# Performance work log

Measured on AMD Instinct MI355X. Metric: run time of the kernel, lower is better.

## Reference

```python
import jax, jax.numpy as jnp
import numpy as np
from jax import lax

B, N, W, L, H = 8, 1024, 1024, 12, 16
EPS = 1e-5


def setup_inputs() -> dict:
    key = jax.random.key(0)
    ks = jax.random.split(key, 14)
    std = 0.25 / np.sqrt(W)  # init_scale * sqrt(1/width)
    inp = {
        "x": jax.random.normal(ks[0], (B, N, W), dtype=jnp.float32),
        # stacked per-layer params, leading dim L
        "ln1_g": jnp.ones((L, W), jnp.float32),
        "ln1_b": jnp.zeros((L, W), jnp.float32),
        "w_qkv": jax.random.normal(ks[1], (L, W, 3 * W), jnp.float32) * std,
        "b_qkv": jnp.zeros((L, 3 * W), jnp.float32),
        "w_o":   jax.random.normal(ks[2], (L, W, W), jnp.float32) * std,
        "b_o":   jnp.zeros((L, W), jnp.float32),
        "ln2_g": jnp.ones((L, W), jnp.float32),
        "ln2_b": jnp.zeros((L, W), jnp.float32),
        "w_fc":  jax.random.normal(ks[3], (L, W, 4 * W), jnp.float32) * std,
        "b_fc":  jnp.zeros((L, 4 * W), jnp.float32),
        "w_pr":  jax.random.normal(ks[4], (L, 4 * W, W), jnp.float32) * std,
        "b_pr":  jnp.zeros((L, W), jnp.float32),
    }
    return inp


def _layernorm(x, g, b):
    mu = jnp.mean(x, axis=-1, keepdims=True)
    var = jnp.mean(jnp.square(x - mu), axis=-1, keepdims=True)
    return (x - mu) * lax.rsqrt(var + EPS) * g + b


def _attention(qkv, heads):
    # qkv: [B, N, 3W]; matches QKVMultiheadAttention exactly
    bs, n_ctx, width3 = qkv.shape
    attn_ch = width3 // heads // 3
    scale = 1.0 / np.sqrt(np.sqrt(attn_ch))
    qkv = qkv.reshape(bs, n_ctx, heads, 3 * attn_ch)
    q, k, v = jnp.split(qkv, 3, axis=-1)  # each [B,N,H,c]
    w = jnp.einsum("bthc,bshc->bhts", q * scale, k * scale)
    w = jax.nn.softmax(w.astype(jnp.float32), axis=-1).astype(qkv.dtype)
    out = jnp.einsum("bhts,bshc->bthc", w, v)
    return out.reshape(bs, n_ctx, heads * attn_ch)


def reference(x, ln1_g, ln1_b, w_qkv, b_qkv, w_o, b_o,
              ln2_g, ln2_b, w_fc, b_fc, w_pr, b_pr):
    params = (ln1_g, ln1_b, w_qkv, b_qkv, w_o, b_o,
              ln2_g, ln2_b, w_fc, b_fc, w_pr, b_pr)

    def step(h, p):
        (g1, bb1, wqkv, bqkv, wo, bo, g2, bb2, wfc, bfc, wpr, bpr) = p
        a = _layernorm(h, g1, bb1)
        a = jnp.einsum("bnw,wk->bnk", a, wqkv) + bqkv
        a = _attention(a, H)
        a = jnp.einsum("bnw,wk->bnk", a, wo) + bo
        h = h + a
        m = _layernorm(h, g2, bb2)
        m = jax.nn.gelu(jnp.einsum("bnw,wf->bnf", m, wfc) + bfc, approximate=False)
        m = jnp.einsum("bnf,fw->bnw", m, wpr) + bpr
        return h + m, None

    out, _ = lax.scan(step, x, params)
    return out
```

## Files before the change

kernel.cpp:

```cpp
#include <hip/hip_runtime.h>
#include <cstdint>
#include <cstddef>

#define WDIM 1024
#define BDIM 8
#define NDIM 1024
#define LDIM 12
#define HDIM 16
#define MROWS (BDIM * NDIM)

using bf16x8 = __attribute__((ext_vector_type(8))) __bf16;
using f32x4  = __attribute__((ext_vector_type(4))) float;
using u32x4  = __attribute__((ext_vector_type(4))) uint32_t;
using u16x8  = __attribute__((ext_vector_type(8))) ushort;

static __device__ __forceinline__ f32x4 mfma16(bf16x8 a, bf16x8 b, f32x4 c) {
  return __builtin_amdgcn_mfma_f32_16x16x32_bf16(a, b, c, 0, 0, 0);
}

static __device__ __forceinline__ ushort f2bf(float f) {
  uint32_t u = __builtin_bit_cast(uint32_t, f);
  u = (u + 0x7FFFu + ((u >> 16) & 1u)) >> 16;
  return (ushort)u;
}

static __device__ __forceinline__ uint32_t cvtpk(float lo, float hi) {
  uint32_t r;
  asm("v_cvt_pk_bf16_f32 %0, %1, %2" : "=v"(r) : "v"(lo), "v"(hi));
  return r;
}

static __device__ __forceinline__ void g2lds16(const void* g, void* l) {
  __builtin_amdgcn_global_load_lds(
      (__attribute__((address_space(1))) void*)(g),
      (__attribute__((address_space(3))) void*)(l), 16, 0, 0);
}

__global__ __launch_bounds__(256) void ln_kernel(const float* __restrict__ h,
                                                 const float* __restrict__ g,
                                                 const float* __restrict__ b,
                                                 ushort* __restrict__ out) {
  const int w = threadIdx.x >> 6, l = threadIdx.x & 63;
  const int row = blockIdx.x * 4 + w;
  const float4* rp = (const float4*)(h + (size_t)row * WDIM);
  float4 v[4];
  float s = 0.f, s2 = 0.f;
  #pragma unroll
  for (int j = 0; j < 4; ++j) {
    v[j] = rp[j * 64 + l];
    s  += v[j].x + v[j].y + v[j].z + v[j].w;
    s2 += v[j].x * v[j].x + v[j].y * v[j].y + v[j].z * v[j].z + v[j].w * v[j].w;
  }
  #pragma unroll
  for (int off = 32; off; off >>= 1) {
    s  += __shfl_xor(s, off);
    s2 += __shfl_xor(s2, off);
  }
  const float mu   = s * (1.0f / WDIM);
  const float var  = s2 * (1.0f / WDIM) - mu * mu;
  const float rstd = rsqrtf(var + 1e-5f);
  ushort4* op = (ushort4*)(out + (size_t)row * WDIM);
  #pragma unroll
  for (int j = 0; j < 4; ++j) {
    const float4 gv = ((const float4*)g)[j * 64 + l];
    const float4 bv = ((const float4*)b)[j * 64 + l];
    ushort4 o;
    o.x = f2bf((v[j].x - mu) * rstd * gv.x + bv.x);
    o.y = f2bf((v[j].y - mu) * rstd * gv.y + bv.y);
    o.z = f2bf((v[j].z - mu) * rstd * gv.z + bv.z);
    o.w = f2bf((v[j].w - mu) * rstd * gv.w + bv.w);
    op[j * 64 + l] = o;
  }
}

__global__ __launch_bounds__(256) void transpose_cvt(const float* __restrict__ in,
                                                     ushort* __restrict__ out,
                                                     int K, int N) {
  __shared__ float sm[32][33];
  const int n0 = blockIdx.x * 32, k0 = blockIdx.y * 32;
  const int tx = threadIdx.x, ty = threadIdx.y;
  #pragma unroll
  for (int j = 0; j < 4; ++j)
    sm[ty + j * 8][tx] = in[(size_t)(k0 + ty + j * 8) * N + n0 + tx];
  __syncthreads();
  #pragma unroll
  for (int j = 0; j < 4; ++j)
    out[(size_t)(n0 + ty + j * 8) * K + k0 + tx] = f2bf(sm[tx][ty + j * 8]);
}

__global__ __launch_bounds__(256) void v_transpose(const ushort* __restrict__ qkv,
                                                   ushort* __restrict__ vT) {
  const int nb = blockIdx.x, bh = blockIdx.y;
  const int b = bh >> 4, h = bh & 15;
  const int tid = threadIdx.x;
  __shared__ ushort smT[64 * 64];
  const int n0 = nb * 64;
  const size_t rowb = (size_t)b * NDIM;
  #pragma unroll
  for (int p = 0; p < 2; ++p) {
    const int n  = p * 32 + (tid >> 3);
    const int d0 = (tid & 7) * 8;
    const uint4 vv = *(const uint4*)(qkv + (rowb + n0 + n) * 3072 + h * 192 + 128 + d0);
    const ushort* e = (const ushort*)&vv;
    const int key = d0;
    #pragma unroll
    for (int j = 0; j < 8; ++j)
      smT[(d0 + j) * 64 + (n ^ key)] = e[j];
  }
  __syncthreads();
  #pragma unroll
  for (int p = 0; p < 2; ++p) {
    const int d  = p * 32 + (tid >> 3);
    const int nc = (tid & 7) * 8;
    const int key = (d >> 3) << 3;
    const uint4 ov = *(const uint4*)&smT[d * 64 + (nc ^ key)];
    *(uint4*)(vT + ((size_t)bh * 64 + d) * NDIM + n0 + nc) = ov;
  }
}

enum { EPI_BF16 = 0, EPI_RES = 1, EPI_GELU = 2 };

template <int EPI>
__global__ __launch_bounds__(512, 2) void gemm256_kernel(
    const ushort* __restrict__ A, const ushort* __restrict__ Bt,
    const float* __restrict__ bias, ushort* __restrict__ outb,
    int M, int N, int K) {
  __shared__ ushort smA[2 * 2 * 256 * 32];
  __shared__ ushort smB[2 * 2 * 256 * 32];
  const int tid = threadIdx.x;
  const int w = tid >> 6, l = tid & 63;
  const int lr = l & 15, lg = l >> 4;
  const int wm = w >> 2, wn = w & 3;

  const int gx = gridDim.x;
  const int nwg = gx * gridDim.y;
  const int id0 = blockIdx.y * gx + blockIdx.x;
  const int id = (id0 & 7) * (nwg >> 3) + (id0 >> 3);
  const int row0 = (id / gx) * 256, col0 = (id % gx) * 256;

  const int KT = K >> 6;
  const int srow_l = l >> 2;
  const int scol = (((l & 3) ^ ((l >> 3) & 3)) * 8);
  const int ks = ((lg ^ ((lr >> 1) & 3)) * 8);

  f32x4 acc[8][4] = {};

  auto stageA = [&](int tau, int hh) {
    const int base = (((tau & 1) * 2 + hh) * 8192);
    const int colb = tau * 64 + hh * 32 + scol;
    #pragma unroll
    for (int j = 0; j < 2; ++j) {
      const int c = j * 8 + w;
      g2lds16(A + (size_t)(row0 + 16 * c + srow_l) * K + colb, &smA[base + c * 512]);
    }
  };
  auto stageB = [&](int tau, int hh) {
    const int base = (((tau & 1) * 2 + hh) * 8192);
    const int colb = tau * 64 + hh * 32 + scol;
    #pragma unroll
    for (int j = 0; j < 2; ++j) {
      const int c = j * 8 + w;
      g2lds16(Bt + (size_t)(col0 + 16 * c + srow_l) * K + colb, &smB[base + c * 512]);
    }
  };

  stageA(0, 0); stageB(0, 0);
  stageA(0, 1); stageB(0, 1);
  stageA(1, 0); stageB(1, 0);
  asm volatile("s_waitcnt vmcnt(8)" ::: "memory");
  __builtin_amdgcn_sched_barrier(0);
  __builtin_amdgcn_s_barrier();

  for (int tau = 0; tau < KT; ++tau) {
    const int ab0 = (tau & 1) * 16384;
    const int ab1 = ab0 + 8192;
    bf16x8 af[8], bf0, bf1;

    #pragma unroll
    for (int m = 0; m < 8; ++m)
      af[m] = *(const bf16x8*)&smA[ab0 + (wm * 128 + m * 16 + lr) * 32 + ks];
    bf0 = *(const bf16x8*)&smB[ab0 + (wn * 64 + lr) * 32 + ks];
    bf1 = *(const bf16x8*)&smB[ab0 + (wn * 64 + 16 + lr) * 32 + ks];
    if (tau + 1 < KT) stageA(tau + 1, 1);
    __builtin_amdgcn_s_barrier();
    asm volatile("s_waitcnt lgkmcnt(0)" ::: "memory");
    __builtin_amdgcn_sched_barrier(0);
    __builtin_amdgcn_s_setprio(1);
    #pragma unroll
    for (int m = 0; m < 8; ++m) {
      acc[m][0] = mfma16(af[m], bf0, acc[m][0]);
      acc[m][1] = mfma16(af[m], bf1, acc[m][1]);
    }
    __builtin_amdgcn_s_setprio(0);
    __builtin_amdgcn_s_barrier();

    bf0 = *(const bf16x8*)&smB[ab0 + (wn * 64 + 32 + lr) * 32 + ks];
    bf1 = *(const bf16x8*)&smB[ab0 + (wn * 64 + 48 + lr) * 32 + ks];
    if (tau + 1 < KT) stageB(tau + 1, 1);
    __builtin_amdgcn_s_barrier();
    asm volatile("s_waitcnt lgkmcnt(0)" ::: "memory");
    __builtin_amdgcn_sched_barrier(0);
    __builtin_amdgcn_s_setprio(1);
    #pragma unroll
    for (int m = 0; m < 8; ++m) {
      acc[m][2] = mfma16(af[m], bf0, acc[m][2]);
      acc[m][3] = mfma16(af[m], bf1, acc[m][3]);
    }
    __builtin_amdgcn_s_setprio(0);
    if (tau + 1 < KT) { asm volatile("s_waitcnt vmcnt(8)" ::: "memory"); }
    else              { asm volatile("s_waitcnt vmcnt(0)" ::: "memory"); }
    __builtin_amdgcn_sched_barrier(0);
    __builtin_amdgcn_s_barrier();

    #pragma unroll
    for (int m = 0; m < 8; ++m)
      af[m] = *(const bf16x8*)&smA[ab1 + (wm * 128 + m * 16 + lr) * 32 + ks];
    bf0 = *(const bf16x8*)&smB[ab1 + (wn * 64 + lr) * 32 + ks];
    bf1 = *(const bf16x8*)&smB[ab1 + (wn * 64 + 16 + lr) * 32 + ks];
    if (tau + 2 < KT) { stageA(tau + 2, 0); stageB(tau + 2, 0); }
    __builtin_amdgcn_s_barrier();
    asm volatile("s_waitcnt lgkmcnt(0)" ::: "memory");
    __builtin_amdgcn_sched_barrier(0);
    __builtin_amdgcn_s_setprio(1);
    #pragma unroll
    for (int m = 0; m < 8; ++m) {
      acc[m][0] = mfma16(af[m], bf0, acc[m][0]);
      acc[m][1] = mfma16(af[m], bf1, acc[m][1]);
    }
    __builtin_amdgcn_s_setprio(0);
    __builtin_amdgcn_s_barrier();

    bf0 = *(const bf16x8*)&smB[ab1 + (wn * 64 + 32 + lr) * 32 + ks];
    bf1 = *(const bf16x8*)&smB[ab1 + (wn * 64 + 48 + lr) * 32 + ks];
    __builtin_amdgcn_s_barrier();
    asm volatile("s_waitcnt lgkmcnt(0)" ::: "memory");
    __builtin_amdgcn_sched_barrier(0);
    __builtin_amdgcn_s_setprio(1);
    #pragma unroll
    for (int m = 0; m < 8; ++m) {
      acc[m][2] = mfma16(af[m], bf0, acc[m][2]);
      acc[m][3] = mfma16(af[m], bf1, acc[m][3]);
    }
    __builtin_amdgcn_s_setprio(0);
    if (tau + 2 < KT)      { asm volatile("s_waitcnt vmcnt(8)" ::: "memory"); }
    else if (tau + 1 < KT) { asm volatile("s_waitcnt vmcnt(4)" ::: "memory"); }
    __builtin_amdgcn_sched_barrier(0);
    __builtin_amdgcn_s_barrier();
  }

  #pragma unroll
  for (int m = 0; m < 8; ++m) {
    #pragma unroll
    for (int n = 0; n < 4; ++n) {
      #pragma unroll
      for (int i = 0; i < 4; ++i) {
        const int r = row0 + wm * 128 + m * 16 + lg * 4 + i;
        const int c = col0 + wn * 64 + n * 16 + lr;
        float v = acc[m][n][i] + bias[c];
        if constexpr (EPI == EPI_GELU) {
          v = 0.5f * v * (1.0f + erff(v * 0.70710678118f));
        }
        outb[(size_t)r * N + c] = f2bf(v);
      }
    }
  }
}

template <int EPI>
__global__ __launch_bounds__(256) void gemm_kernel(
    const ushort* __restrict__ A, const ushort* __restrict__ Bt,
    const float* __restrict__ bias, float* __restrict__ resid,
    ushort* __restrict__ outb, int M, int N, int K) {
  __shared__ ushort smA[2][128 * 64];
  __shared__ ushort smB[2][128 * 64];
  const int tid = threadIdx.x;
  const int w = tid >> 6, l = tid & 63;
  const int lr = l & 15, lg = l >> 4;
  const int wr = (w >> 1) * 64, wc = (w & 1) * 64;

  const int gx = gridDim.x;
  const int nwg = gx * gridDim.y;
  const int id0 = blockIdx.y * gx + blockIdx.x;
  const int id = (id0 & 7) * (nwg >> 3) + (id0 >> 3);
  const int row0 = (id / gx) * 128, col0 = (id % gx) * 128;

  const int srow = tid >> 3;
  const int sslot = tid & 7;
  f32x4 acc[4][4] = {};
  const int KT = K >> 6;

  auto stage = [&](int buf, int kt) {
    const int kb = kt << 6;
    #pragma unroll
    for (int j = 0; j < 4; ++j) {
      const int r = j * 32 + srow;
      const int sc = ((sslot ^ (r & 7)) * 8);
      g2lds16(A  + (size_t)(row0 + r) * K + kb + sc, &smA[buf][j * 2048 + w * 512]);
      g2lds16(Bt + (size_t)(col0 + r) * K + kb + sc, &smB[buf][j * 2048 + w * 512]);
    }
  };

  stage(0, 0);
  int cur = 0;
  for (int kt = 0; kt < KT; ++kt) {
    __syncthreads();
    if (kt + 1 < KT) stage(cur ^ 1, kt + 1);
    bf16x8 af[2][4], bfr[2][4];
    const int rs = lr & 7;
    #pragma unroll
    for (int kk = 0; kk < 2; ++kk) {
      #pragma unroll
      for (int t = 0; t < 4; ++t) {
        const int k8 = (kk * 4 + lg) ^ rs;
        af[kk][t]  = *(const bf16x8*)&smA[cur][(wr + t * 16 + lr) * 64 + k8 * 8];
        bfr[kk][t] = *(const bf16x8*)&smB[cur][(wc + t * 16 + lr) * 64 + k8 * 8];
      }
    }
    __builtin_amdgcn_s_setprio(1);
    #pragma unroll
    for (int kk = 0; kk < 2; ++kk)
      #pragma unroll
      for (int mt = 0; mt < 4; ++mt)
        #pragma unroll
        for (int nt = 0; nt < 4; ++nt)
          acc[mt][nt] = mfma16(af[kk][mt], bfr[kk][nt], acc[mt][nt]);
    __builtin_amdgcn_s_setprio(0);
    cur ^= 1;
  }

  #pragma unroll
  for (int mt = 0; mt < 4; ++mt) {
    #pragma unroll
    for (int nt = 0; nt < 4; ++nt) {
      #pragma unroll
      for (int i = 0; i < 4; ++i) {
        const int r = row0 + wr + mt * 16 + lg * 4 + i;
        const int c = col0 + wc + nt * 16 + lr;
        float v = acc[mt][nt][i] + bias[c];
        if constexpr (EPI == EPI_RES) {
          resid[(size_t)r * N + c] += v;
        } else if constexpr (EPI == EPI_GELU) {
          const float gg = 0.5f * v * (1.0f + erff(v * 0.70710678118f));
          outb[(size_t)r * N + c] = f2bf(gg);
        } else {
          outb[(size_t)r * N + c] = f2bf(v);
        }
      }
    }
  }
}

__global__ __launch_bounds__(512) void attn_kernel(const ushort* __restrict__ qkv,
                                                   const ushort* __restrict__ vT,
                                                   ushort* __restrict__ out) {
  const int qb = blockIdx.x;
  const int bh = blockIdx.y;
  const int b = bh >> 4, h = bh & 15;
  const int tid = threadIdx.x;
  const int w = tid >> 6, l = tid & 63;
  const int lr = l & 15, lg = l >> 4;
  __shared__ ushort smK[2][64 * 64];
  __shared__ ushort smV[2][64 * 64];
  const int q0 = qb * 128 + w * 16;
  const size_t rowb = (size_t)b * NDIM;
  const ushort* vhead = vT + (size_t)bh * 64 * NDIM;

  const u16x8 ob = {0x3F80, 0x3F80, 0x3F80, 0x3F80, 0x3F80, 0x3F80, 0x3F80, 0x3F80};
  const bf16x8 onesv = __builtin_bit_cast(bf16x8, ob);

  const int srow = l >> 3;
  const int skey = (srow & 3) ^ ((w & 1) << 2);
  const int scol = ((l & 7) ^ skey) * 8;
  const ushort* kg = qkv + (rowb + w * 8 + srow) * 3072 + h * 192 + 64 + scol;
  const ushort* vg = vhead + (size_t)(w * 8 + srow) * NDIM + scol;

  auto stage = [&](int buf, int kb) {
    g2lds16(kg + (size_t)kb * 64 * 3072, &smK[buf][w * 512]);
    g2lds16(vg + kb * 64,                &smV[buf][w * 512]);
  };

  bf16x8 qf0, qf1;
  {
    const ushort* qp = qkv + (rowb + q0 + lr) * 3072 + h * 192;
    qf0 = *(const bf16x8*)(qp + lg * 8);
    qf1 = *(const bf16x8*)(qp + 32 + lg * 8);
  }
  f32x4 o[4] = {};
  f32x4 lacc = {0.f, 0.f, 0.f, 0.f};

  const int rbase = (lr >> 2) * 8 + (lr & 3);
  const int kkey  = (lr & 3) ^ (((lr >> 2) & 1) << 2);
  const int vkey  = (lr & 3) ^ (((lr >> 3) & 1) << 2);
  const int kp0 = (lg ^ kkey) * 8, kp1 = ((4 + lg) ^ kkey) * 8;
  const int vp0 = (lg ^ vkey) * 8, vp1 = ((4 + lg) ^ vkey) * 8;

  stage(0, 0);
  int cur = 0;
  for (int kb = 0; kb < NDIM / 64; ++kb) {
    __syncthreads();
    if (kb + 1 < NDIM / 64) stage(cur ^ 1, kb + 1);

    f32x4 s[2][2];
    #pragma unroll
    for (int hh = 0; hh < 2; ++hh) {
      #pragma unroll
      for (int m = 0; m < 2; ++m) {
        const int r = hh * 32 + rbase + 4 * m;
        const ushort* kr = &smK[cur][r * 64];
        const bf16x8 kf0 = *(const bf16x8*)&kr[kp0];
        const bf16x8 kf1 = *(const bf16x8*)&kr[kp1];
        f32x4 z = {0.f, 0.f, 0.f, 0.f};
        s[hh][m] = mfma16(kf1, qf1, mfma16(kf0, qf0, z));
      }
    }

    bf16x8 pf[2];
    #pragma unroll
    for (int hh = 0; hh < 2; ++hh) {
      u32x4 pk;
      pk[0] = cvtpk(__expf(s[hh][0][0] * 0.125f), __expf(s[hh][0][1] * 0.125f));
      pk[1] = cvtpk(__expf(s[hh][0][2] * 0.125f), __expf(s[hh][0][3] * 0.125f));
      pk[2] = cvtpk(__expf(s[hh][1][0] * 0.125f), __expf(s[hh][1][1] * 0.125f));
      pk[3] = cvtpk(__expf(s[hh][1][2] * 0.125f), __expf(s[hh][1][3] * 0.125f));
      pf[hh] = __builtin_bit_cast(bf16x8, pk);
    }

    lacc = mfma16(pf[0], onesv, mfma16(pf[1], onesv, lacc));
    #pragma unroll
    for (int dt = 0; dt < 4; ++dt) {
      const ushort* vrow = &smV[cur][(dt * 16 + lr) * 64];
      const bf16x8 vf0 = *(const bf16x8*)&vrow[vp0];
      const bf16x8 vf1 = *(const bf16x8*)&vrow[vp1];
      o[dt] = mfma16(pf[0], vf0, mfma16(pf[1], vf1, o[dt]));
    }
    cur ^= 1;
  }

  #pragma unroll
  for (int i = 0; i < 4; ++i) {
    const float inv = 1.0f / lacc[i];
    const size_t orow = (rowb + q0 + lg * 4 + i) * (size_t)WDIM;
    #pragma unroll
    for (int dt = 0; dt < 4; ++dt)
      out[orow + h * 64 + dt * 16 + lr] = f2bf(o[dt][i] * inv);
  }
}

extern "C" void kernel_launch(void* const* d_in, const int* in_sizes, int n_in,
                              void* d_out, int out_size, void* d_ws, size_t ws_size,
                              hipStream_t stream) {
  const float* x     = (const float*)d_in[0];
  const float* ln1_g = (const float*)d_in[1];
  const float* ln1_b = (const float*)d_in[2];
  const float* w_qkv = (const float*)d_in[3];
  const float* b_qkv = (const float*)d_in[4];
  const float* w_o   = (const float*)d_in[5];
  const float* b_o   = (const float*)d_in[6];
  const float* ln2_g = (const float*)d_in[7];
  const float* ln2_b = (const float*)d_in[8];
  const float* w_fc  = (const float*)d_in[9];
  const float* b_fc  = (const float*)d_in[10];
  const float* w_pr  = (const float*)d_in[11];
  const float* b_pr  = (const float*)d_in[12];

  float* hbuf = (float*)d_out;

  uint8_t* p = (uint8_t*)d_ws;
  ushort* wqkv_t = (ushort*)p; p += (size_t)3072 * 1024 * 2;
  ushort* wo_t   = (ushort*)p; p += (size_t)1024 * 1024 * 2;
  ushort* wfc_t  = (ushort*)p; p += (size_t)4096 * 1024 * 2;
  ushort* wpr_t  = (ushort*)p; p += (size_t)1024 * 4096 * 2;
  ushort* lnb    = (ushort*)p; p += (size_t)MROWS * 1024 * 2;
  ushort* qkvb   = (ushort*)p; p += (size_t)MROWS * 3072 * 2;
  ushort* attnb  = (ushort*)p; p += (size_t)MROWS * 1024 * 2;
  ushort* mlpb   = (ushort*)p; p += (size_t)MROWS * 4096 * 2;
  ushort* vTb    = (ushort*)p; p += (size_t)BDIM * HDIM * 64 * NDIM * 2;

  hipMemcpyAsync(hbuf, x, (size_t)MROWS * WDIM * sizeof(float),
                 hipMemcpyDeviceToDevice, stream);

  for (int l = 0; l < LDIM; ++l) {
    ln_kernel<<<MROWS / 4, 256, 0, stream>>>(hbuf, ln1_g + l * 1024, ln1_b + l * 1024, lnb);
    transpose_cvt<<<dim3(96, 32), dim3(32, 8), 0, stream>>>(
        w_qkv + (size_t)l * 1024 * 3072, wqkv_t, 1024, 3072);
    gemm256_kernel<EPI_BF16><<<dim3(12, 32), 512, 0, stream>>>(
        lnb, wqkv_t, b_qkv + (size_t)l * 3072, qkvb, MROWS, 3072, 1024);
    v_transpose<<<dim3(16, 128), 256, 0, stream>>>(qkvb, vTb);
    attn_kernel<<<dim3(8, 128), 512, 0, stream>>>(qkvb, vTb, attnb);
    transpose_cvt<<<dim3(32, 32), dim3(32, 8), 0, stream>>>(
        w_o + (size_t)l * 1024 * 1024, wo_t, 1024, 1024);
    gemm_kernel<EPI_RES><<<dim3(8, 64), 256, 0, stream>>>(
        attnb, wo_t, b_o + (size_t)l * 1024, hbuf, nullptr, MROWS, 1024, 1024);
    ln_kernel<<<MROWS / 4, 256, 0, stream>>>(hbuf, ln2_g + l * 1024, ln2_b + l * 1024, lnb);
    transpose_cvt<<<dim3(128, 32), dim3(32, 8), 0, stream>>>(
        w_fc + (size_t)l * 1024 * 4096, wfc_t, 1024, 4096);
    gemm256_kernel<EPI_GELU><<<dim3(16, 32), 512, 0, stream>>>(
        lnb, wfc_t, b_fc + (size_t)l * 4096, mlpb, MROWS, 4096, 1024);
    transpose_cvt<<<dim3(32, 128), dim3(32, 8), 0, stream>>>(
        w_pr + (size_t)l * 4096 * 1024, wpr_t, 4096, 1024);
    gemm_kernel<EPI_RES><<<dim3(8, 64), 256, 0, stream>>>(
        mlpb, wpr_t, b_pr + (size_t)l * 1024, hbuf, nullptr, MROWS, 1024, 4096);
  }
}
```

Before: 4.442 ms.

## Route residual GEMMs through 256-tile kernel with split-K atomic accumulation

```diff
diff --git a/kernel.cpp b/kernel.cpp
--- a/kernel.cpp
+++ b/kernel.cpp
@@ -118,13 +118,13 @@
   }
 }
 
-enum { EPI_BF16 = 0, EPI_RES = 1, EPI_GELU = 2 };
+enum { EPI_BF16 = 0, EPI_RESA = 1, EPI_GELU = 2 };
 
 template <int EPI>
 __global__ __launch_bounds__(512, 2) void gemm256_kernel(
     const ushort* __restrict__ A, const ushort* __restrict__ Bt,
-    const float* __restrict__ bias, ushort* __restrict__ outb,
-    int M, int N, int K) {
+    const float* __restrict__ bias, float* __restrict__ resid,
+    ushort* __restrict__ outb, int M, int N, int Kfull, int Kslice) {
   __shared__ ushort smA[2 * 2 * 256 * 32];
   __shared__ ushort smB[2 * 2 * 256 * 32];
   const int tid = threadIdx.x;
@@ -132,13 +132,17 @@
   const int lr = l & 15, lg = l >> 4;
   const int wm = w >> 2, wn = w & 3;
 
+  const int z = blockIdx.z;
+  const ushort* Ab  = A  + (size_t)z * Kslice;
+  const ushort* Btb = Bt + (size_t)z * Kslice;
+
   const int gx = gridDim.x;
   const int nwg = gx * gridDim.y;
   const int id0 = blockIdx.y * gx + blockIdx.x;
   const int id = (id0 & 7) * (nwg >> 3) + (id0 >> 3);
   const int row0 = (id / gx) * 256, col0 = (id % gx) * 256;
 
-  const int KT = K >> 6;
+  const int KT = Kslice >> 6;
   const int srow_l = l >> 2;
   const int scol = (((l & 3) ^ ((l >> 3) & 3)) * 8);
   const int ks = ((lg ^ ((lr >> 1) & 3)) * 8);
@@ -151,7 +155,7 @@
     #pragma unroll
     for (int j = 0; j < 2; ++j) {
       const int c = j * 8 + w;
-      g2lds16(A + (size_t)(row0 + 16 * c + srow_l) * K + colb, &smA[base + c * 512]);
+      g2lds16(Ab + (size_t)(row0 + 16 * c + srow_l) * Kfull + colb, &smA[base + c * 512]);
     }
   };
   auto stageB = [&](int tau, int hh) {
@@ -160,7 +164,7 @@
     #pragma unroll
     for (int j = 0; j < 2; ++j) {
       const int c = j * 8 + w;
-      g2lds16(Bt + (size_t)(col0 + 16 * c + srow_l) * K + colb, &smB[base + c * 512]);
+      g2lds16(Btb + (size_t)(col0 + 16 * c + srow_l) * Kfull + colb, &smB[base + c * 512]);
     }
   };
 
@@ -256,93 +260,14 @@
       for (int i = 0; i < 4; ++i) {
         const int r = row0 + wm * 128 + m * 16 + lg * 4 + i;
         const int c = col0 + wn * 64 + n * 16 + lr;
-        float v = acc[m][n][i] + bias[c];
-        if constexpr (EPI == EPI_GELU) {
-          v = 0.5f * v * (1.0f + erff(v * 0.70710678118f));
-        }
-        outb[(size_t)r * N + c] = f2bf(v);
-      }
-    }
-  }
-}
-
-template <int EPI>
-__global__ __launch_bounds__(256) void gemm_kernel(
-    const ushort* __restrict__ A, const ushort* __restrict__ Bt,
-    const float* __restrict__ bias, float* __restrict__ resid,
-    ushort* __restrict__ outb, int M, int N, int K) {
-  __shared__ ushort smA[2][128 * 64];
-  __shared__ ushort smB[2][128 * 64];
-  const int tid = threadIdx.x;
-  const int w = tid >> 6, l = tid & 63;
-  const int lr = l & 15, lg = l >> 4;
-  const int wr = (w >> 1) * 64, wc = (w & 1) * 64;
-
-  const int gx = gridDim.x;
-  const int nwg = gx * gridDim.y;
-  const int id0 = blockIdx.y * gx + blockIdx.x;
-  const int id = (id0 & 7) * (nwg >> 3) + (id0 >> 3);
-  const int row0 = (id / gx) * 128, col0 = (id % gx) * 128;
-
-  const int srow = tid >> 3;
-  const int sslot = tid & 7;
-  f32x4 acc[4][4] = {};
-  const int KT = K >> 6;
-
-  auto stage = [&](int buf, int kt) {
-    const int kb = kt << 6;
-    #pragma unroll
-    for (int j = 0; j < 4; ++j) {
-      const int r = j * 32 + srow;
-      const int sc = ((sslot ^ (r & 7)) * 8);
-      g2lds16(A  + (size_t)(row0 + r) * K + kb + sc, &smA[buf][j * 2048 + w * 512]);
-      g2lds16(Bt + (size_t)(col0 + r) * K + kb + sc, &smB[buf][j * 2048 + w * 512]);
-    }
-  };
-
-  stage(0, 0);
-  int cur = 0;
-  for (int kt = 0; kt < KT; ++kt) {
-    __syncthreads();
-    if (kt + 1 < KT) stage(cur ^ 1, kt + 1);
-    bf16x8 af[2][4], bfr[2][4];
-    const int rs = lr & 7;
-    #pragma unroll
-    for (int kk = 0; kk < 2; ++kk) {
-      #pragma unroll
-      for (int t = 0; t < 4; ++t) {
-        const int k8 = (kk * 4 + lg) ^ rs;
-        af[kk][t]  = *(const bf16x8*)&smA[cur][(wr + t * 16 + lr) * 64 + k8 * 8];
-        bfr[kk][t] = *(const bf16x8*)&smB[cur][(wc + t * 16 + lr) * 64 + k8 * 8];
-      }
-    }
-    __builtin_amdgcn_s_setprio(1);
-    #pragma unroll
-    for (int kk = 0; kk < 2; ++kk)
-      #pragma unroll
-      for (int mt = 0; mt < 4; ++mt)
-        #pragma unroll
-        for (int nt = 0; nt < 4; ++nt)
-          acc[mt][nt] = mfma16(af[kk][mt], bfr[kk][nt], acc[mt][nt]);
-    __builtin_amdgcn_s_setprio(0);
-    cur ^= 1;
-  }
-
-  #pragma unroll
-  for (int mt = 0; mt < 4; ++mt) {
-    #pragma unroll
-    for (int nt = 0; nt < 4; ++nt) {
-      #pragma unroll
-      for (int i = 0; i < 4; ++i) {
-        const int r = row0 + wr + mt * 16 + lg * 4 + i;
-        const int c = col0 + wc + nt * 16 + lr;
-        float v = acc[mt][nt][i] + bias[c];
-        if constexpr (EPI == EPI_RES) {
-          resid[(size_t)r * N + c] += v;
-        } else if constexpr (EPI == EPI_GELU) {
-          const float gg = 0.5f * v * (1.0f + erff(v * 0.70710678118f));
-          outb[(size_t)r * N + c] = f2bf(gg);
+        if constexpr (EPI == EPI_RESA) {
+          const float v = acc[m][n][i] + (z == 0 ? bias[c] : 0.0f);
+          atomicAdd(&resid[(size_t)r * N + c], v);
         } else {
+          float v = acc[m][n][i] + bias[c];
+          if constexpr (EPI == EPI_GELU) {
+            v = 0.5f * v * (1.0f + erff(v * 0.70710678118f));
+          }
           outb[(size_t)r * N + c] = f2bf(v);
         }
       }
@@ -483,22 +408,22 @@
     ln_kernel<<<MROWS / 4, 256, 0, stream>>>(hbuf, ln1_g + l * 1024, ln1_b + l * 1024, lnb);
     transpose_cvt<<<dim3(96, 32), dim3(32, 8), 0, stream>>>(
         w_qkv + (size_t)l * 1024 * 3072, wqkv_t, 1024, 3072);
-    gemm256_kernel<EPI_BF16><<<dim3(12, 32), 512, 0, stream>>>(
-        lnb, wqkv_t, b_qkv + (size_t)l * 3072, qkvb, MROWS, 3072, 1024);
+    gemm256_kernel<EPI_BF16><<<dim3(12, 32, 1), 512, 0, stream>>>(
+        lnb, wqkv_t, b_qkv + (size_t)l * 3072, nullptr, qkvb, MROWS, 3072, 1024, 1024);
     v_transpose<<<dim3(16, 128), 256, 0, stream>>>(qkvb, vTb);
     attn_kernel<<<dim3(8, 128), 512, 0, stream>>>(qkvb, vTb, attnb);
     transpose_cvt<<<dim3(32, 32), dim3(32, 8), 0, stream>>>(
         w_o + (size_t)l * 1024 * 1024, wo_t, 1024, 1024);
-    gemm_kernel<EPI_RES><<<dim3(8, 64), 256, 0, stream>>>(
-        attnb, wo_t, b_o + (size_t)l * 1024, hbuf, nullptr, MROWS, 1024, 1024);
+    gemm256_kernel<EPI_RESA><<<dim3(4, 32, 2), 512, 0, stream>>>(
+        attnb, wo_t, b_o + (size_t)l * 1024, hbuf, nullptr, MROWS, 1024, 1024, 512);
     ln_kernel<<<MROWS / 4, 256, 0, stream>>>(hbuf, ln2_g + l * 1024, ln2_b + l * 1024, lnb);
     transpose_cvt<<<dim3(128, 32), dim3(32, 8), 0, stream>>>(
         w_fc + (size_t)l * 1024 * 4096, wfc_t, 1024, 4096);
-    gemm256_kernel<EPI_GELU><<<dim3(16, 32), 512, 0, stream>>>(
-        lnb, wfc_t, b_fc + (size_t)l * 4096, mlpb, MROWS, 4096, 1024);
+    gemm256_kernel<EPI_GELU><<<dim3(16, 32, 1), 512, 0, stream>>>(
+        lnb, wfc_t, b_fc + (size_t)l * 4096, nullptr, mlpb, MROWS, 4096, 1024, 1024);
     transpose_cvt<<<dim3(32, 128), dim3(32, 8), 0, stream>>>(
         w_pr + (size_t)l * 4096 * 1024, wpr_t, 4096, 1024);
-    gemm_kernel<EPI_RES><<<dim3(8, 64), 256, 0, stream>>>(
-        mlpb, wpr_t, b_pr + (size_t)l * 1024, hbuf, nullptr, MROWS, 1024, 4096);
-  }
-}
+    gemm256_kernel<EPI_RESA><<<dim3(4, 32, 2), 512, 0, stream>>>(
+        mlpb, wpr_t, b_pr + (size_t)l * 1024, hbuf, nullptr, MROWS, 1024, 4096, 2048);
+  }
+}
```

After: 5.309 ms. 1.2x slower.
